# Kernel optimization log

Hardware: AMD Instinct MI355X
Metric: run time of the kernel (lower is better)

## Reference

```python
import jax, jax.numpy as jnp
from jax import lax
import numpy as np

WS = 5  # window_size
H = 6   # hidden_size
IN = 3 * WS  # 15
OUT = 2


def setup_inputs() -> dict:
    key = jax.random.key(0)
    k1, k2, k3, k4, k5 = jax.random.split(key, 5)
    B, T = 8192, 1024
    one_full_traj = jax.random.normal(k1, (B, T, 3), dtype=jnp.float32)
    # nn.Linear-style params: y = x @ W.T + b
    W1 = jax.random.normal(k2, (H, IN), dtype=jnp.float32) * (1.0 / np.sqrt(IN))
    b1 = jax.random.normal(k3, (H,), dtype=jnp.float32) * 0.05
    W2 = jax.random.normal(k4, (OUT, H), dtype=jnp.float32) * (1.0 / np.sqrt(H))
    b2 = jax.random.normal(k5, (OUT,), dtype=jnp.float32) * 0.05
    return {"one_full_traj": one_full_traj, "W1": W1, "b1": b1, "W2": W2, "b2": b2}


def reference(one_full_traj, W1, b1, W2, b2):
    ws = WS
    B, T, _ = one_full_traj.shape

    def mlp(x):  # [B, 3*ws] -> [B, 2]
        return jnp.tanh(x @ W1.T + b1) @ W2.T + b2

    def make_inp(seq):  # [B, ws, 3] -> [B, 3*ws], channel-major per original cat order
        return jnp.transpose(seq, (0, 2, 1)).reshape(B, 3 * ws)

    # step 0
    out = mlp(make_inp(one_full_traj[:, :ws, :]))[:, None, :]  # [B, 1, 2]

    # warm-up loop t = 1 .. ws-1 (small fixed Python loop, matches original indexing)
    for t in range(1, ws):
        n = out.shape[1]  # == t
        tmp = jnp.concatenate(
            [one_full_traj[:, ws + (t - 1):ws + (t - 1) + n, 0:1], out], axis=2
        )  # [B, t, 3]
        seq = jnp.concatenate([one_full_traj[:, t:ws, :], tmp], axis=1)  # [B, ws, 3]
        out = jnp.concatenate([out, mlp(make_inp(seq))[:, None, :]], axis=1)

    # sliding window of the last ws predictions as carry.
    u = one_full_traj[:, :, 0]  # control channel, [B, T]

    def step(win, t):
        uw = lax.dynamic_slice_in_dim(u, t, ws, axis=1)  # [B, ws]
        seq = jnp.concatenate([uw[:, :, None], win], axis=2)  # [B, ws, 3]
        pred = mlp(make_inp(seq))  # [B, 2]
        win = jnp.concatenate([win[:, 1:, :], pred[:, None, :]], axis=1)
        return win, pred

    ts = jnp.arange(ws, T - ws)
    _, preds = lax.scan(step, out, ts)  # preds: [T-2*ws, B, 2]
    return jnp.concatenate([out, jnp.transpose(preds, (1, 0, 2))], axis=1)  # [B, T-ws, 2]
```

## Files before the change

kernel.cpp:

```cpp
#include <hip/hip_runtime.h>
#include <math.h>

#define TLEN  1024
#define NSTEP 1019

template <int CTRL>
__device__ __forceinline__ float dpp_add(float v) {
    union { int i; float f; } in, out;
    in.f = v;
    out.i = __builtin_amdgcn_update_dpp(0, in.i, CTRL, 0xF, 0xF, false);
    return v + out.f;
}
__device__ __forceinline__ float sum8(float v) {
    v = dpp_add<0xB1>(v);
    v = dpp_add<0x4E>(v);
    v = dpp_add<0x141>(v);
    return v;
}

__device__ __forceinline__ float fast_exp2(float z) {
#if __has_builtin(__builtin_amdgcn_exp2f)
    return __builtin_amdgcn_exp2f(z);
#else
    return exp2f(z);
#endif
}

__global__ __launch_bounds__(64) void MLP_or_nextstep_kernel(
    const float* __restrict__ traj,
    const float* __restrict__ W1,
    const float* __restrict__ b1,
    const float* __restrict__ W2,
    const float* __restrict__ b2,
    float* __restrict__ out)
{
    __shared__ float lds_u[TLEN][8];

    const int lane = threadIdx.x;
    const int g    = lane >> 3;
    const int n    = lane & 7;
    const int bstart = blockIdx.x * 8;
    const int b = bstart + g;

    const float* __restrict__ base = traj + (size_t)b * (TLEN * 3);
    float2* outb = (float2*)out + (size_t)b * NSTEP;
    const bool is_store_lane = (n == 0);

    {
        const int s_elem = lane & 7;
        const int s_row  = lane >> 3;
        const float* __restrict__ sbase = traj + (size_t)(bstart + s_elem) * (TLEN * 3);
        for (int j = 0; j < TLEN / 8; ++j) {
            const float* gp = sbase + (size_t)(8 * j + s_row) * 3;
            __builtin_amdgcn_global_load_lds(
                (const __attribute__((address_space(1))) void*)gp,
                (__attribute__((address_space(3))) void*)&lds_u[8 * j][0],
                4, 0, 0);
        }
    }

    const float KK = 2.8853900817779268f;
    const int nr = (n < 6) ? n : 5;
    float w1row[15], b1r;
#pragma unroll
    for (int j = 0; j < 15; ++j) w1row[j] = KK * W1[nr * 15 + j];
    b1r = KK * b1[nr];
    const float w2a_l = (n < 6) ? W2[n]     : 0.0f;
    const float w2b_l = (n < 6) ? W2[6 + n] : 0.0f;
    const float bias_a = (n == 6) ? b2[0] : 0.0f;
    const float bias_b = (n == 7) ? b2[1] : 0.0f;
    const float c1a = -2.0f * w2a_l, c0a = w2a_l + bias_a;
    const float c1b = -2.0f * w2b_l, c0b = w2b_l + bias_b;

    auto mlp = [&](const float* __restrict__ x, float& ya, float& yb) {
        float z0 = w1row[0] * x[0];
        float z1 = w1row[5] * x[5];
        float z2 = fmaf(w1row[10], x[10], b1r);
#pragma unroll
        for (int j = 1; j < 5; ++j) {
            z0 = fmaf(w1row[j],      x[j],      z0);
            z1 = fmaf(w1row[5 + j],  x[5 + j],  z1);
            z2 = fmaf(w1row[10 + j], x[10 + j], z2);
        }
        float z = (z0 + z1) + z2;
        float r = __builtin_amdgcn_rcpf(fast_exp2(z) + 1.0f);
        ya = sum8(fmaf(c1a, r, c0a));
        yb = sum8(fmaf(c1b, r, c0b));
    };

    float uu[12], vv[5], wc[5];
#pragma unroll
    for (int i = 0; i < 12; ++i) uu[i] = base[i * 3];
#pragma unroll
    for (int i = 0; i < 5; ++i) { vv[i] = base[i * 3 + 1]; wc[i] = base[i * 3 + 2]; }

    float pa[5], pb[5];
    {
        float x[15] = {uu[0],uu[1],uu[2],uu[3],uu[4],
                       vv[0],vv[1],vv[2],vv[3],vv[4],
                       wc[0],wc[1],wc[2],wc[3],wc[4]};
        mlp(x, pa[0], pb[0]);
    }
    {
        float x[15] = {uu[1],uu[2],uu[3],uu[4],uu[5],
                       vv[1],vv[2],vv[3],vv[4],pa[0],
                       wc[1],wc[2],wc[3],wc[4],pb[0]};
        mlp(x, pa[1], pb[1]);
    }
    {
        float x[15] = {uu[2],uu[3],uu[4],uu[6],uu[7],
                       vv[2],vv[3],vv[4],pa[0],pa[1],
                       wc[2],wc[3],wc[4],pb[0],pb[1]};
        mlp(x, pa[2], pb[2]);
    }
    {
        float x[15] = {uu[3],uu[4],uu[7],uu[8],uu[9],
                       vv[3],vv[4],pa[0],pa[1],pa[2],
                       wc[3],wc[4],pb[0],pb[1],pb[2]};
        mlp(x, pa[3], pb[3]);
    }
    {
        float x[15] = {uu[4],uu[8],uu[9],uu[10],uu[11],
                       vv[4],pa[0],pa[1],pa[2],pa[3],
                       wc[4],pb[0],pb[1],pb[2],pb[3]};
        mlp(x, pa[4], pb[4]);
    }
    if (is_store_lane) {
#pragma unroll
        for (int i = 0; i < 5; ++i) outb[i] = make_float2(pa[i], pb[i]);
    }

    __syncthreads();

    float aw[5], bw[5];
#pragma unroll
    for (int i = 0; i < 5; ++i) { aw[i] = pa[i]; bw[i] = pb[i]; }

    const float* up  = &lds_u[5][g];
    const float* upn;
    float2* sp = outb + n + 5;
    float unA[9], unB[9];

#pragma unroll
    for (int i = 0; i < 9; ++i) unA[i] = up[8 * i];
    upn = up + 40;

#define LOADN(BUF)                                                           \
    {                                                                        \
        _Pragma("unroll")                                                    \
        for (int i = 0; i < 9; ++i) BUF[i] = upn[8 * i];                     \
        upn += 40;                                                           \
    }

    float duC[5], duD[5];
#pragma unroll
    for (int i = 0; i < 5; ++i) {
        float d = w1row[0] * unA[i];
        d = fmaf(w1row[1], unA[i + 1], d);
        d = fmaf(w1row[2], unA[i + 2], d);
        d = fmaf(w1row[3], unA[i + 3], d);
        d = fmaf(w1row[4], unA[i + 4], d);
        duC[i] = d;
    }

    LOADN(unB)

    float pAc, pBc, pAn, pBn;
    pAc = w1row[5] * aw[0];
    pAc = fmaf(w1row[6], aw[1], pAc);
    pAc = fmaf(w1row[7], aw[2], pAc);
    pAc = fmaf(w1row[8], aw[3], pAc);
    pBc = fmaf(w1row[10], bw[0], b1r);
    pBc = fmaf(w1row[11], bw[1], pBc);
    pBc = fmaf(w1row[12], bw[2], pBc);
    pBc = fmaf(w1row[13], bw[3], pBc);

#define STEP(S, DUC, DUN, UN, J, M)                                          \
    {                                                                        \
        float tA = fmaf(w1row[9],  aw[((S) + 4) % 5], pAc);                  \
        float tB = fmaf(w1row[14], bw[((S) + 4) % 5], pBc);                  \
        float z  = (DUC[S] + tA) + tB;                                       \
        float e  = fast_exp2(z);                                             \
             \
        pAn = w1row[5] * aw[((S) + 1) % 5];                                  \
        pAn = fmaf(w1row[6], aw[((S) + 2) % 5], pAn);                        \
        pAn = fmaf(w1row[7], aw[((S) + 3) % 5], pAn);                        \
        pAn = fmaf(w1row[8], aw[((S) + 4) % 5], pAn);                        \
        pBn = fmaf(w1row[10], bw[((S) + 1) % 5], b1r);                       \
        pBn = fmaf(w1row[11], bw[((S) + 2) % 5], pBn);                       \
        pBn = fmaf(w1row[12], bw[((S) + 3) % 5], pBn);                       \
        pBn = fmaf(w1row[13], bw[((S) + 4) % 5], pBn);                       \
        {                                                                    \
            float d = w1row[0] * UN[S];                                      \
            d = fmaf(w1row[1], UN[(S) + 1], d);                              \
            d = fmaf(w1row[2], UN[(S) + 2], d);                              \
            d = fmaf(w1row[3], UN[(S) + 3], d);                              \
            d = fmaf(w1row[4], UN[(S) + 4], d);                              \
            DUN[S] = d;                                                      \
        }                                                                    \
                                        \
        float r  = __builtin_amdgcn_rcpf(e + 1.0f);                          \
        float ya = sum8(fmaf(c1a, r, c0a));                                  \
        float yb = sum8(fmaf(c1b, r, c0b));                                  \
        if (n == (J)) { ka##M = ya; kb##M = yb; }                            \
        aw[(S) % 5] = ya; bw[(S) % 5] = yb;                                  \
        pAc = pAn; pBc = pBn;                                                \
    }

#define STORE(M) sp[8 * (M)] = make_float2(ka##M, kb##M);

    for (int sb = 0; sb < 25; ++sb) {
        float ka0 = 0, kb0 = 0, ka1 = 0, kb1 = 0, ka2 = 0, kb2 = 0,
              ka3 = 0, kb3 = 0, ka4 = 0, kb4 = 0;
        LOADN(unA)
        STEP(0, duC, duD, unB, 0, 0) STEP(1, duC, duD, unB, 1, 0) STEP(2, duC, duD, unB, 2, 0)
        STEP(3, duC, duD, unB, 3, 0) STEP(4, duC, duD, unB, 4, 0)
        LOADN(unB)
        STEP(0, duD, duC, unA, 5, 0) STEP(1, duD, duC, unA, 6, 0) STEP(2, duD, duC, unA, 7, 0) STORE(0)
        STEP(3, duD, duC, unA, 0, 1) STEP(4, duD, duC, unA, 1, 1)
        LOADN(unA)
        STEP(0, duC, duD, unB, 2, 1) STEP(1, duC, duD, unB, 3, 1) STEP(2, duC, duD, unB, 4, 1)
        STEP(3, duC, duD, unB, 5, 1) STEP(4, duC, duD, unB, 6, 1)
        LOADN(unB)
        STEP(0, duD, duC, unA, 7, 1) STORE(1)
        STEP(1, duD, duC, unA, 0, 2) STEP(2, duD, duC, unA, 1, 2) STEP(3, duD, duC, unA, 2, 2) STEP(4, duD, duC, unA, 3, 2)
        LOADN(unA)
        STEP(0, duC, duD, unB, 4, 2) STEP(1, duC, duD, unB, 5, 2) STEP(2, duC, duD, unB, 6, 2)
        STEP(3, duC, duD, unB, 7, 2) STORE(2)
        STEP(4, duC, duD, unB, 0, 3)
        LOADN(unB)
        STEP(0, duD, duC, unA, 1, 3) STEP(1, duD, duC, unA, 2, 3) STEP(2, duD, duC, unA, 3, 3)
        STEP(3, duD, duC, unA, 4, 3) STEP(4, duD, duC, unA, 5, 3)
        LOADN(unA)
        STEP(0, duC, duD, unB, 6, 3) STEP(1, duC, duD, unB, 7, 3) STORE(3)
        STEP(2, duC, duD, unB, 0, 4) STEP(3, duC, duD, unB, 1, 4) STEP(4, duC, duD, unB, 2, 4)
        LOADN(unB)
        STEP(0, duD, duC, unA, 3, 4) STEP(1, duD, duC, unA, 4, 4) STEP(2, duD, duC, unA, 5, 4)
        STEP(3, duD, duC, unA, 6, 4) STEP(4, duD, duC, unA, 7, 4) STORE(4)

        sp += 40;
    }

    float2* tp = outb + 1005;
#define TSTEP(S, UN, K)                                                      \
    {                                                                        \
        float z0 = w1row[0] * UN[S];                                         \
        float z1 = w1row[5] * aw[(S) % 5];                                   \
        float z2 = fmaf(w1row[10], bw[(S) % 5], b1r);                        \
        z0 = fmaf(w1row[1], UN[(S) + 1], z0);                                \
        z1 = fmaf(w1row[6], aw[((S) + 1) % 5], z1);                          \
        z2 = fmaf(w1row[11], bw[((S) + 1) % 5], z2);                         \
        z0 = fmaf(w1row[2], UN[(S) + 2], z0);                                \
        z1 = fmaf(w1row[7], aw[((S) + 2) % 5], z1);                          \
        z2 = fmaf(w1row[12], bw[((S) + 2) % 5], z2);                         \
        z0 = fmaf(w1row[3], UN[(S) + 3], z0);                                \
        z1 = fmaf(w1row[8], aw[((S) + 3) % 5], z1);                          \
        z2 = fmaf(w1row[13], bw[((S) + 3) % 5], z2);                         \
        z0 = fmaf(w1row[4], UN[(S) + 4], z0);                                \
        z1 = fmaf(w1row[9], aw[((S) + 4) % 5], z1);                          \
        z2 = fmaf(w1row[14], bw[((S) + 4) % 5], z2);                         \
        float z = (z0 + z1) + z2;                                            \
        float r = __builtin_amdgcn_rcpf(fast_exp2(z) + 1.0f);                \
        float ya = sum8(fmaf(c1a, r, c0a));                                  \
        float yb = sum8(fmaf(c1b, r, c0b));                                  \
        if (is_store_lane) tp[K] = make_float2(ya, yb);                      \
        aw[(S) % 5] = ya; bw[(S) % 5] = yb;                                  \
    }

    TSTEP(0, unA, 0) TSTEP(1, unA, 1) TSTEP(2, unA, 2) TSTEP(3, unA, 3) TSTEP(4, unA, 4)
    LOADN(unA)
    TSTEP(0, unB, 5) TSTEP(1, unB, 6) TSTEP(2, unB, 7) TSTEP(3, unB, 8) TSTEP(4, unB, 9)
    TSTEP(0, unA, 10) TSTEP(1, unA, 11) TSTEP(2, unA, 12) TSTEP(3, unA, 13)

#undef TSTEP
#undef STORE
#undef STEP
#undef LOADN
}

extern "C" void kernel_launch(void* const* d_in, const int* in_sizes, int n_in,
                              void* d_out, int out_size, void* d_ws, size_t ws_size,
                              hipStream_t stream) {
    const float* traj = (const float*)d_in[0];
    const float* W1   = (const float*)d_in[1];
    const float* b1   = (const float*)d_in[2];
    const float* W2   = (const float*)d_in[3];
    const float* b2   = (const float*)d_in[4];
    float* out = (float*)d_out;

    const int grid = 8192 / 8;
    MLP_or_nextstep_kernel<<<grid, 64, 0, stream>>>(traj, W1, b1, W2, b2, out);
}
```

Measured before the change: 238.7 us.

## Split each batch row across two 8-lane halves, one per output channel

Each trajectory now gets 16 lanes instead of 8. Each 8-lane half computes the reduction for only one of the two outputs, and the halves swap results with a row-shift DPP. This halves the batch rows per wave (4 instead of 8), doubles the grid, and shrinks the LDS staging buffer. The aim is a shorter serial per-step critical path (one sum8 instead of two) in exchange for twice the waves and redundant hidden-layer work in each half. The risk is that the extra cross-half DPP and select add latency to each step.

```diff
diff --git a/kernel.cpp b/kernel.cpp
--- a/kernel.cpp
+++ b/kernel.cpp
@@ -16,6 +16,12 @@
     v = dpp_add<0x4E>(v);
     v = dpp_add<0x141>(v);
     return v;
+}
+__device__ __forceinline__ float xhalf(float v) {
+    union { int i; float f; } in, out;
+    in.f = v;
+    out.i = __builtin_amdgcn_update_dpp(0, in.i, 0x128, 0xF, 0xF, false);
+    return out.f;
 }
 
 __device__ __forceinline__ float fast_exp2(float z) {
@@ -34,27 +40,31 @@
     const float* __restrict__ b2,
     float* __restrict__ out)
 {
-    __shared__ float lds_u[TLEN][8];
+    __shared__ float lds_u[TLEN][4];
 
     const int lane = threadIdx.x;
-    const int g    = lane >> 3;
+    const int e    = lane >> 4;
+    const int h    = (lane >> 3) & 1;
     const int n    = lane & 7;
-    const int bstart = blockIdx.x * 8;
-    const int b = bstart + g;
+    const int nh   = lane & 15;
+    const int bstart = blockIdx.x * 4;
+    const int b = bstart + e;
 
     const float* __restrict__ base = traj + (size_t)b * (TLEN * 3);
     float2* outb = (float2*)out + (size_t)b * NSTEP;
-    const bool is_store_lane = (n == 0);
-
-    {
-        const int s_elem = lane & 7;
-        const int s_row  = lane >> 3;
+    const bool is_store_lane = (nh == 0);
+    const bool stl  = (h == 0);
+    const bool hsel = (h == 1);
+
+    {
+        const int s_elem = lane & 3;
+        const int s_row  = lane >> 2;
         const float* __restrict__ sbase = traj + (size_t)(bstart + s_elem) * (TLEN * 3);
-        for (int j = 0; j < TLEN / 8; ++j) {
-            const float* gp = sbase + (size_t)(8 * j + s_row) * 3;
+        for (int j = 0; j < TLEN / 16; ++j) {
+            const float* gp = sbase + (size_t)(16 * j + s_row) * 3;
             __builtin_amdgcn_global_load_lds(
                 (const __attribute__((address_space(1))) void*)gp,
-                (__attribute__((address_space(3))) void*)&lds_u[8 * j][0],
+                (__attribute__((address_space(3))) void*)&lds_u[16 * j][0],
                 4, 0, 0);
         }
     }
@@ -65,12 +75,9 @@
 #pragma unroll
     for (int j = 0; j < 15; ++j) w1row[j] = KK * W1[nr * 15 + j];
     b1r = KK * b1[nr];
-    const float w2a_l = (n < 6) ? W2[n]     : 0.0f;
-    const float w2b_l = (n < 6) ? W2[6 + n] : 0.0f;
-    const float bias_a = (n == 6) ? b2[0] : 0.0f;
-    const float bias_b = (n == 7) ? b2[1] : 0.0f;
-    const float c1a = -2.0f * w2a_l, c0a = w2a_l + bias_a;
-    const float c1b = -2.0f * w2b_l, c0b = w2b_l + bias_b;
+    const float w2_l  = (n < 6) ? W2[h * 6 + n] : 0.0f;
+    const float bias  = (n == 6) ? b2[h] : 0.0f;
+    const float c1 = -2.0f * w2_l, c0 = w2_l + bias;
 
     auto mlp = [&](const float* __restrict__ x, float& ya, float& yb) {
         float z0 = w1row[0] * x[0];
@@ -84,8 +91,10 @@
         }
         float z = (z0 + z1) + z2;
         float r = __builtin_amdgcn_rcpf(fast_exp2(z) + 1.0f);
-        ya = sum8(fmaf(c1a, r, c0a));
-        yb = sum8(fmaf(c1b, r, c0b));
+        float own = sum8(fmaf(c1, r, c0));
+        float oth = xhalf(own);
+        ya = hsel ? oth : own;
+        yb = hsel ? own : oth;
     };
 
     float uu[12], vv[5], wc[5];
@@ -136,20 +145,20 @@
 #pragma unroll
     for (int i = 0; i < 5; ++i) { aw[i] = pa[i]; bw[i] = pb[i]; }
 
-    const float* up  = &lds_u[5][g];
+    const float* up  = &lds_u[5][e];
     const float* upn;
     float2* sp = outb + n + 5;
     float unA[9], unB[9];
 
 #pragma unroll
-    for (int i = 0; i < 9; ++i) unA[i] = up[8 * i];
-    upn = up + 40;
+    for (int i = 0; i < 9; ++i) unA[i] = up[4 * i];
+    upn = up + 20;
 
 #define LOADN(BUF)                                                           \
     {                                                                        \
         _Pragma("unroll")                                                    \
-        for (int i = 0; i < 9; ++i) BUF[i] = upn[8 * i];                     \
-        upn += 40;                                                           \
+        for (int i = 0; i < 9; ++i) BUF[i] = upn[4 * i];                     \
+        upn += 20;                                                           \
     }
 
     float duC[5], duD[5];
@@ -180,7 +189,7 @@
         float tA = fmaf(w1row[9],  aw[((S) + 4) % 5], pAc);                  \
         float tB = fmaf(w1row[14], bw[((S) + 4) % 5], pBc);                  \
         float z  = (DUC[S] + tA) + tB;                                       \
-        float e  = fast_exp2(z);                                             \
+        float ex = fast_exp2(z);                                             \
              \
         pAn = w1row[5] * aw[((S) + 1) % 5];                                  \
         pAn = fmaf(w1row[6], aw[((S) + 2) % 5], pAn);                        \
@@ -199,15 +208,17 @@
             DUN[S] = d;                                                      \
         }                                                                    \
                                         \
-        float r  = __builtin_amdgcn_rcpf(e + 1.0f);                          \
-        float ya = sum8(fmaf(c1a, r, c0a));                                  \
-        float yb = sum8(fmaf(c1b, r, c0b));                                  \
-        if (n == (J)) { ka##M = ya; kb##M = yb; }                            \
+        float r  = __builtin_amdgcn_rcpf(ex + 1.0f);                         \
+        float own = sum8(fmaf(c1, r, c0));                                   \
+        float oth = xhalf(own);                                              \
+        float ya = hsel ? oth : own;                                         \
+        float yb = hsel ? own : oth;                                         \
+        if (nh == (J)) { ka##M = ya; kb##M = yb; }                           \
         aw[(S) % 5] = ya; bw[(S) % 5] = yb;                                  \
         pAc = pAn; pBc = pBn;                                                \
     }
 
-#define STORE(M) sp[8 * (M)] = make_float2(ka##M, kb##M);
+#define STORE(M) if (stl) sp[8 * (M)] = make_float2(ka##M, kb##M);
 
     for (int sb = 0; sb < 25; ++sb) {
         float ka0 = 0, kb0 = 0, ka1 = 0, kb1 = 0, ka2 = 0, kb2 = 0,
@@ -261,8 +272,10 @@
         z2 = fmaf(w1row[14], bw[((S) + 4) % 5], z2);                         \
         float z = (z0 + z1) + z2;                                            \
         float r = __builtin_amdgcn_rcpf(fast_exp2(z) + 1.0f);                \
-        float ya = sum8(fmaf(c1a, r, c0a));                                  \
-        float yb = sum8(fmaf(c1b, r, c0b));                                  \
+        float own = sum8(fmaf(c1, r, c0));                                   \
+        float oth = xhalf(own);                                              \
+        float ya = hsel ? oth : own;                                         \
+        float yb = hsel ? own : oth;                                         \
         if (is_store_lane) tp[K] = make_float2(ya, yb);                      \
         aw[(S) % 5] = ya; bw[(S) % 5] = yb;                                  \
     }
@@ -288,6 +301,6 @@
     const float* b2   = (const float*)d_in[4];
     float* out = (float*)d_out;
 
-    const int grid = 8192 / 8;
+    const int grid = 8192 / 4;
     MLP_or_nextstep_kernel<<<grid, 64, 0, stream>>>(traj, W1, b1, W2, b2, out);
 }
```

Result: slower. 274.4 us (+15.0%).
